# Performance work log

Hardware: AMD Instinct MI355X
Metric: run time of the kernel (lower is better)

## Reference

```python
import jax, jax.numpy as jnp
import numpy as np

LOG2 = float(np.log(2.0))
E, G, F, C = 500000, 64, 128, 4

def shifted_softplus(x):
    return jax.nn.softplus(x) - LOG2

def setup_inputs() -> dict:
    key = jax.random.key(0)
    ks = jax.random.split(key, 6)
    return {
        "edge_attr": jax.random.normal(ks[0], (E, G), dtype=jnp.float32),
        "colors": jax.random.randint(ks[1], (E,), 0, C),
        "W1": jax.random.normal(ks[2], (C, G, F), dtype=jnp.float32) * (1.0 / np.sqrt(G)),
        "b1": jax.random.normal(ks[3], (C, F), dtype=jnp.float32) * 0.01,
        "W2": jax.random.normal(ks[4], (C, F, F), dtype=jnp.float32) * (1.0 / np.sqrt(F)),
        "b2": jax.random.normal(ks[5], (C, F), dtype=jnp.float32) * 0.01,
    }

def reference(edge_attr, colors, W1, b1, W2, b2):
    # Apply every color-expert MLP to all edges, then select per-edge expert output.
    # Faithful to the torch loop: out[colors==i] = mlp_i(edge_attr[colors==i]).
    # h: [C, E, F]
    h = jnp.einsum('eg,cgf->cef', edge_attr, W1) + b1[:, None, :]
    h = shifted_softplus(h)
    y = jnp.einsum('cef,cfh->ceh', h, W2) + b2[:, None, :]  # [C, E, F]
    out = y[colors, jnp.arange(E)]  # [E, F] select each edge's own color expert
    return out
```

## Files before the change

kernel.cpp:

```cpp
#include <hip/hip_runtime.h>
#include <hip/hip_bf16.h>

#define G_DIM 64
#define F_DIM 128
#define C_DIM 4
#define NB    512

#define META_COUNTS 0
#define META_BASES  4
#define META_TSTART 9
#define BH_OFF      32
#define IDX_OFF     (32 + NB*C_DIM)

typedef __bf16 bf16x8 __attribute__((ext_vector_type(8)));
typedef float  f32x4  __attribute__((ext_vector_type(4)));

__device__ inline unsigned short f2bf(float f) {
    union { float f; unsigned u; } v; v.f = f;
    unsigned r = v.u + 0x7FFFu + ((v.u >> 16) & 1u);
    return (unsigned short)(r >> 16);
}

__device__ inline float ssp(float x) {
    float t = __expf(-fabsf(x));
    return fmaxf(x, 0.f) + __logf(1.f + t) - 0.69314718055994531f;
}

__global__ void k_prep1(const int* __restrict__ colors, int E, int CH,
                        unsigned* __restrict__ bh,
                        const float* __restrict__ W1, const float* __restrict__ W2,
                        unsigned short* __restrict__ w1t, unsigned short* __restrict__ w2t) {
    int tid = threadIdx.x;
    if (blockIdx.x < NB) {
        __shared__ unsigned h[C_DIM];
        if (tid < C_DIM) h[tid] = 0;
        __syncthreads();
        int lo = blockIdx.x * CH, hi = lo + CH; if (hi > E) hi = E;
        int lane = tid & 63;
        for (int i0 = lo; i0 < hi; i0 += 256) {
            int i = i0 + tid;
            int c = (i < hi) ? colors[i] : -1;
#pragma unroll
            for (int cc = 0; cc < C_DIM; ++cc) {
                unsigned long long m = __ballot(c == cc);
                if (lane == 0 && m) atomicAdd(&h[cc], (unsigned)__popcll(m));
            }
        }
        __syncthreads();
        if (tid < C_DIM) bh[blockIdx.x * C_DIM + tid] = h[tid];
    } else {
        int i = (blockIdx.x - NB) * 256 + tid;
        if (i < C_DIM * F_DIM * G_DIM) {
            int k = i % G_DIM, n = (i / G_DIM) % F_DIM, c = i / (G_DIM * F_DIM);
            w1t[i] = f2bf(W1[(c * G_DIM + k) * F_DIM + n]);
        }
        if (i < C_DIM * F_DIM * F_DIM) {
            int k = i % F_DIM, n = (i / F_DIM) % F_DIM, c = i / (F_DIM * F_DIM);
            w2t[i] = f2bf(W2[(c * F_DIM + k) * F_DIM + n]);
        }
    }
}

__global__ void k_prep2(const int* __restrict__ colors, int E, int CH,
                        const unsigned* __restrict__ bh, unsigned* __restrict__ meta,
                        int* __restrict__ idx) {
    __shared__ unsigned cur[C_DIM], tmpb[C_DIM], tot[C_DIM];
    int tid = threadIdx.x, w = tid >> 6, lane = tid & 63;

    unsigned run = 0;
    for (int b0 = 0; b0 < NB; b0 += 64) {
        int b = b0 + lane;
        unsigned v = bh[b * C_DIM + w];
        unsigned s = v;
#pragma unroll
        for (int d = 1; d < 64; d <<= 1) {
            unsigned t = __shfl_up(s, d, 64);
            if (lane >= d) s += t;
        }
        if (b == (int)blockIdx.x) tmpb[w] = run + s - v;
        run += __shfl(s, 63, 64);
    }
    if (lane == 0) tot[w] = run;
    __syncthreads();
    if (blockIdx.x == 0 && tid == 0) {
        unsigned bsum = 0, tsum = 0;
#pragma unroll
        for (int c = 0; c < C_DIM; ++c) {
            meta[META_BASES + c] = bsum;
            meta[META_COUNTS + c] = tot[c];
            meta[META_TSTART + c] = tsum;
            bsum += tot[c];
            tsum += (tot[c] + 63) >> 6;
        }
        meta[META_BASES + C_DIM] = bsum;
        meta[META_TSTART + C_DIM] = tsum;
    }
    if (lane == 0) {
        unsigned cb = 0;
        for (int c = 0; c < w; ++c) cb += tot[c];
        cur[w] = tmpb[w] + cb;
    }
    __syncthreads();

    int lo = blockIdx.x * CH, hi = lo + CH; if (hi > E) hi = E;
    for (int i0 = lo; i0 < hi; i0 += 256) {
        int i = i0 + tid;
        int c = (i < hi) ? colors[i] : -1;
#pragma unroll
        for (int cc = 0; cc < C_DIM; ++cc) {
            unsigned long long m = __ballot(c == cc);
            if (!m) continue;
            int leader = __ffsll(m) - 1;
            unsigned base = 0;
            if (lane == leader) base = atomicAdd(&cur[cc], (unsigned)__popcll(m));
            base = __shfl(base, leader, 64);
            if (c == cc) {
                unsigned off = __popcll(m & ((1ull << lane) - 1ull));
                idx[base + off] = i;
            }
        }
    }
}

__global__ __launch_bounds__(256, 6) void mlp_main(
    const float* __restrict__ ea, const float* __restrict__ b1,
    const float* __restrict__ b2, const unsigned short* __restrict__ w1t,
    const unsigned short* __restrict__ w2t, const unsigned* __restrict__ meta,
    const int* __restrict__ idx, float* __restrict__ out) {
    __shared__ __align__(16) unsigned short A[64][72];
    __shared__ __align__(16) unsigned short H[64][136];
    __shared__ int rowmap[64];

    unsigned b = blockIdx.x;
    if (b >= meta[META_TSTART + C_DIM]) return;
    int c = 0;
    if (b >= meta[META_TSTART + 1]) c = 1;
    if (b >= meta[META_TSTART + 2]) c = 2;
    if (b >= meta[META_TSTART + 3]) c = 3;
    int t = (int)(b - meta[META_TSTART + c]);
    int segBase = (int)meta[META_BASES + c];
    int segCnt  = (int)meta[META_COUNTS + c];
    int row0 = t * 64;
    int nrows = segCnt - row0; if (nrows > 64) nrows = 64;

    int tid = threadIdx.x;
    if (tid < 64) rowmap[tid] = (tid < nrows) ? idx[segBase + row0 + tid] : -1;
    __syncthreads();

    {
        int r = tid >> 2, q = tid & 3;
        int e = rowmap[r];
        unsigned short tmp[16];
        if (e >= 0) {
            const float4* src = (const float4*)(ea + (size_t)e * G_DIM + q * 16);
#pragma unroll
            for (int i = 0; i < 4; ++i) {
                float4 v = src[i];
                tmp[i * 4 + 0] = f2bf(v.x); tmp[i * 4 + 1] = f2bf(v.y);
                tmp[i * 4 + 2] = f2bf(v.z); tmp[i * 4 + 3] = f2bf(v.w);
            }
        } else {
#pragma unroll
            for (int i = 0; i < 16; ++i) tmp[i] = 0;
        }
        *(uint4*)&A[r][q * 16]     = *(uint4*)&tmp[0];
        *(uint4*)&A[r][q * 16 + 8] = *(uint4*)&tmp[8];
    }

    int w = tid >> 6, lane = tid & 63;
    int l15 = lane & 15, l4 = lane >> 4;

    bf16x8 fB1[2][2]; float bias1[2];
#pragma unroll
    for (int nt = 0; nt < 2; ++nt) {
        int n = w * 32 + nt * 16 + l15;
        bias1[nt] = b1[c * F_DIM + n];
#pragma unroll
        for (int ks = 0; ks < 2; ++ks)
            fB1[nt][ks] = *(const bf16x8*)(w1t + ((size_t)(c * F_DIM + n) * G_DIM + ks * 32 + l4 * 8));
    }
    __syncthreads();

    f32x4 acc[4][2];
#pragma unroll
    for (int mt = 0; mt < 4; ++mt)
#pragma unroll
        for (int nt = 0; nt < 2; ++nt) acc[mt][nt] = (f32x4){0.f, 0.f, 0.f, 0.f};
#pragma unroll
    for (int ks = 0; ks < 2; ++ks) {
#pragma unroll
        for (int mt = 0; mt < 4; ++mt) {
            bf16x8 a = *(const bf16x8*)&A[mt * 16 + l15][ks * 32 + l4 * 8];
            acc[mt][0] = __builtin_amdgcn_mfma_f32_16x16x32_bf16(a, fB1[0][ks], acc[mt][0], 0, 0, 0);
            acc[mt][1] = __builtin_amdgcn_mfma_f32_16x16x32_bf16(a, fB1[1][ks], acc[mt][1], 0, 0, 0);
        }
    }

#pragma unroll
    for (int mt = 0; mt < 4; ++mt)
#pragma unroll
        for (int nt = 0; nt < 2; ++nt)
#pragma unroll
            for (int r = 0; r < 4; ++r) {
                float v = acc[mt][nt][r] + bias1[nt];
                H[mt * 16 + l4 * 4 + r][w * 32 + nt * 16 + l15] = f2bf(ssp(v));
            }

    bf16x8 fB2[2][4]; float bias2[2];
#pragma unroll
    for (int nt = 0; nt < 2; ++nt) {
        int n = w * 32 + nt * 16 + l15;
        bias2[nt] = b2[c * F_DIM + n];
#pragma unroll
        for (int ks = 0; ks < 4; ++ks)
            fB2[nt][ks] = *(const bf16x8*)(w2t + ((size_t)(c * F_DIM + n) * F_DIM + ks * 32 + l4 * 8));
    }
    __syncthreads();

#pragma unroll
    for (int mt = 0; mt < 4; ++mt)
#pragma unroll
        for (int nt = 0; nt < 2; ++nt) acc[mt][nt] = (f32x4){0.f, 0.f, 0.f, 0.f};
#pragma unroll
    for (int ks = 0; ks < 4; ++ks) {
#pragma unroll
        for (int mt = 0; mt < 4; ++mt) {
            bf16x8 a = *(const bf16x8*)&H[mt * 16 + l15][ks * 32 + l4 * 8];
            acc[mt][0] = __builtin_amdgcn_mfma_f32_16x16x32_bf16(a, fB2[0][ks], acc[mt][0], 0, 0, 0);
            acc[mt][1] = __builtin_amdgcn_mfma_f32_16x16x32_bf16(a, fB2[1][ks], acc[mt][1], 0, 0, 0);
        }
    }

#pragma unroll
    for (int mt = 0; mt < 4; ++mt) {
#pragma unroll
        for (int r = 0; r < 4; ++r) {
            int e = rowmap[mt * 16 + l4 * 4 + r];
            if (e >= 0) {
                float* p = out + (size_t)e * F_DIM + w * 32 + l15;
                __builtin_nontemporal_store(acc[mt][0][r] + bias2[0], p);
                __builtin_nontemporal_store(acc[mt][1][r] + bias2[1], p + 16);
            }
        }
    }
}

__global__ void fallback(const float* __restrict__ ea, const int* __restrict__ colors,
                         const float* __restrict__ W1, const float* __restrict__ b1,
                         const float* __restrict__ W2, const float* __restrict__ b2,
                         float* __restrict__ out, int E) {
    __shared__ float sh[4][F_DIM + G_DIM];
    int w = threadIdx.x >> 6, lane = threadIdx.x & 63;
    int e = blockIdx.x * 4 + w;
    bool valid = (e < E);
    int ec = valid ? e : 0;
    int c = colors[ec];
    float* hv = sh[w];
    float* av = sh[w] + F_DIM;
    av[lane] = ea[(size_t)ec * G_DIM + lane];
    __syncthreads();
    for (int f = lane; f < F_DIM; f += 64) {
        float s = b1[c * F_DIM + f];
        for (int g = 0; g < G_DIM; ++g) s += av[g] * W1[(c * G_DIM + g) * F_DIM + f];
        hv[f] = ssp(s);
    }
    __syncthreads();
    for (int f = lane; f < F_DIM; f += 64) {
        float s = b2[c * F_DIM + f];
        for (int k = 0; k < F_DIM; ++k) s += hv[k] * W2[(c * F_DIM + k) * F_DIM + f];
        if (valid) out[(size_t)e * F_DIM + f] = s;
    }
}

extern "C" void kernel_launch(void* const* d_in, const int* in_sizes, int n_in,
                              void* d_out, int out_size, void* d_ws, size_t ws_size,
                              hipStream_t stream) {
    const float* ea     = (const float*)d_in[0];
    const int*   colors = (const int*)d_in[1];
    const float* W1     = (const float*)d_in[2];
    const float* b1     = (const float*)d_in[3];
    const float* W2     = (const float*)d_in[4];
    const float* b2     = (const float*)d_in[5];
    float* out = (float*)d_out;
    int E = in_sizes[1];

    size_t need = (size_t)(IDX_OFF + E) * 4 +
                  (size_t)(C_DIM * F_DIM * G_DIM + C_DIM * F_DIM * F_DIM) * 2;
    if (ws_size < need) {
        int blocks = (E + 3) / 4;
        fallback<<<blocks, 256, 0, stream>>>(ea, colors, W1, b1, W2, b2, out, E);
        return;
    }

    unsigned* meta = (unsigned*)d_ws;
    unsigned* bh   = (unsigned*)d_ws + BH_OFF;
    int* idx = (int*)d_ws + IDX_OFF;
    unsigned short* w1t = (unsigned short*)((char*)d_ws + (size_t)(IDX_OFF + E) * 4);
    unsigned short* w2t = w1t + C_DIM * F_DIM * G_DIM;

    int CH = (E + NB - 1) / NB;
    k_prep1<<<NB + 256, 256, 0, stream>>>(colors, E, CH, bh, W1, W2, w1t, w2t);
    k_prep2<<<NB, 256, 0, stream>>>(colors, E, CH, bh, meta, idx);
    int g = (E + 63) / 64 + C_DIM;
    mlp_main<<<g, 256, 0, stream>>>(ea, b1, b2, w1t, w2t, meta, idx, out);
}
```

Before: 92.24 us.

## Give each wave its own 16-row tile and drop block barriers and shared A staging

Changes the work split so each wave owns 16 rows across all 128 output features instead of 32 columns across all 64 rows. The A fragment is loaded from global straight into registers, and each wave keeps a private H slice, so the rowmap and A shared tiles and all __syncthreads go away. The cost is that every wave now loads the full W1 and W2 slices per tile (four times the weight traffic per block, mostly cache hits), and launch bounds drop from 6 to 4 blocks to leave more registers.

After: 212.4 us. 130% more time.

```diff
diff --git a/kernel.cpp b/kernel.cpp
--- a/kernel.cpp
+++ b/kernel.cpp
@@ -122,14 +122,12 @@
     }
 }
 
-__global__ __launch_bounds__(256, 6) void mlp_main(
+__global__ __launch_bounds__(256, 4) void mlp_main(
     const float* __restrict__ ea, const float* __restrict__ b1,
     const float* __restrict__ b2, const unsigned short* __restrict__ w1t,
     const unsigned short* __restrict__ w2t, const unsigned* __restrict__ meta,
     const int* __restrict__ idx, float* __restrict__ out) {
-    __shared__ __align__(16) unsigned short A[64][72];
-    __shared__ __align__(16) unsigned short H[64][136];
-    __shared__ int rowmap[64];
+    __shared__ __align__(16) unsigned short H[4][16][136];
 
     unsigned b = blockIdx.x;
     if (b >= meta[META_TSTART + C_DIM]) return;
@@ -141,105 +139,90 @@
     int segBase = (int)meta[META_BASES + c];
     int segCnt  = (int)meta[META_COUNTS + c];
     int row0 = t * 64;
-    int nrows = segCnt - row0; if (nrows > 64) nrows = 64;
-
-    int tid = threadIdx.x;
-    if (tid < 64) rowmap[tid] = (tid < nrows) ? idx[segBase + row0 + tid] : -1;
-    __syncthreads();
-
+
+    int tid = threadIdx.x, w = tid >> 6, lane = tid & 63;
+    int l15 = lane & 15, l4 = lane >> 4;
+
+    int rloc = w * 16 + l15;
+    bool av = rloc < (segCnt - row0);
+    int e_a = av ? idx[segBase + row0 + rloc] : -1;
+    int e_safe = av ? e_a : 0;
+
+    int es[4];
+#pragma unroll
+    for (int r = 0; r < 4; ++r) es[r] = __shfl(e_a, l4 * 4 + r, 64);
+
+    bf16x8 aF[2];
     {
-        int r = tid >> 2, q = tid & 3;
-        int e = rowmap[r];
-        unsigned short tmp[16];
-        if (e >= 0) {
-            const float4* src = (const float4*)(ea + (size_t)e * G_DIM + q * 16);
-#pragma unroll
-            for (int i = 0; i < 4; ++i) {
-                float4 v = src[i];
-                tmp[i * 4 + 0] = f2bf(v.x); tmp[i * 4 + 1] = f2bf(v.y);
-                tmp[i * 4 + 2] = f2bf(v.z); tmp[i * 4 + 3] = f2bf(v.w);
-            }
-        } else {
-#pragma unroll
-            for (int i = 0; i < 16; ++i) tmp[i] = 0;
-        }
-        *(uint4*)&A[r][q * 16]     = *(uint4*)&tmp[0];
-        *(uint4*)&A[r][q * 16 + 8] = *(uint4*)&tmp[8];
-    }
-
-    int w = tid >> 6, lane = tid & 63;
-    int l15 = lane & 15, l4 = lane >> 4;
-
-    bf16x8 fB1[2][2]; float bias1[2];
-#pragma unroll
-    for (int nt = 0; nt < 2; ++nt) {
-        int n = w * 32 + nt * 16 + l15;
-        bias1[nt] = b1[c * F_DIM + n];
-#pragma unroll
-        for (int ks = 0; ks < 2; ++ks)
-            fB1[nt][ks] = *(const bf16x8*)(w1t + ((size_t)(c * F_DIM + n) * G_DIM + ks * 32 + l4 * 8));
-    }
-    __syncthreads();
-
-    f32x4 acc[4][2];
-#pragma unroll
-    for (int mt = 0; mt < 4; ++mt)
-#pragma unroll
-        for (int nt = 0; nt < 2; ++nt) acc[mt][nt] = (f32x4){0.f, 0.f, 0.f, 0.f};
-#pragma unroll
-    for (int ks = 0; ks < 2; ++ks) {
-#pragma unroll
-        for (int mt = 0; mt < 4; ++mt) {
-            bf16x8 a = *(const bf16x8*)&A[mt * 16 + l15][ks * 32 + l4 * 8];
-            acc[mt][0] = __builtin_amdgcn_mfma_f32_16x16x32_bf16(a, fB1[0][ks], acc[mt][0], 0, 0, 0);
-            acc[mt][1] = __builtin_amdgcn_mfma_f32_16x16x32_bf16(a, fB1[1][ks], acc[mt][1], 0, 0, 0);
-        }
-    }
-
-#pragma unroll
-    for (int mt = 0; mt < 4; ++mt)
-#pragma unroll
-        for (int nt = 0; nt < 2; ++nt)
+        const float* src = ea + (size_t)e_safe * G_DIM + l4 * 8;
+#pragma unroll
+        for (int ks = 0; ks < 2; ++ks) {
+            float4 v0 = *(const float4*)(src + ks * 32);
+            float4 v1 = *(const float4*)(src + ks * 32 + 4);
+            union { bf16x8 b; unsigned short u[8]; } tv;
+            tv.u[0] = f2bf(v0.x); tv.u[1] = f2bf(v0.y);
+            tv.u[2] = f2bf(v0.z); tv.u[3] = f2bf(v0.w);
+            tv.u[4] = f2bf(v1.x); tv.u[5] = f2bf(v1.y);
+            tv.u[6] = f2bf(v1.z); tv.u[7] = f2bf(v1.w);
+            aF[ks] = tv.b;
+        }
+    }
+
+#pragma unroll
+    for (int nh = 0; nh < 2; ++nh) {
+        f32x4 acc[4];
+#pragma unroll
+        for (int nt = 0; nt < 4; ++nt) acc[nt] = (f32x4){0.f, 0.f, 0.f, 0.f};
+#pragma unroll
+        for (int nt = 0; nt < 4; ++nt) {
+            int n = nh * 64 + nt * 16 + l15;
+            const unsigned short* wp = w1t + (size_t)(c * F_DIM + n) * G_DIM + l4 * 8;
+            bf16x8 fb0 = *(const bf16x8*)(wp);
+            bf16x8 fb1 = *(const bf16x8*)(wp + 32);
+            acc[nt] = __builtin_amdgcn_mfma_f32_16x16x32_bf16(aF[0], fb0, acc[nt], 0, 0, 0);
+            acc[nt] = __builtin_amdgcn_mfma_f32_16x16x32_bf16(aF[1], fb1, acc[nt], 0, 0, 0);
+        }
+#pragma unroll
+        for (int nt = 0; nt < 4; ++nt) {
+            int n = nh * 64 + nt * 16 + l15;
+            float bias = b1[c * F_DIM + n];
+#pragma unroll
+            for (int r = 0; r < 4; ++r)
+                H[w][l4 * 4 + r][n] = f2bf(ssp(acc[nt][r] + bias));
+        }
+    }
+
+    asm volatile("s_waitcnt lgkmcnt(0)" ::: "memory");
+
+    bf16x8 ha[4];
+#pragma unroll
+    for (int ks = 0; ks < 4; ++ks)
+        ha[ks] = *(const bf16x8*)&H[w][l15][ks * 32 + l4 * 8];
+
+#pragma unroll
+    for (int nh = 0; nh < 2; ++nh) {
+        f32x4 acc[4];
+#pragma unroll
+        for (int nt = 0; nt < 4; ++nt) acc[nt] = (f32x4){0.f, 0.f, 0.f, 0.f};
+#pragma unroll
+        for (int nt = 0; nt < 4; ++nt) {
+            int n = nh * 64 + nt * 16 + l15;
+            const unsigned short* wp = w2t + (size_t)(c * F_DIM + n) * F_DIM + l4 * 8;
+#pragma unroll
+            for (int ks = 0; ks < 4; ++ks) {
+                bf16x8 fb = *(const bf16x8*)(wp + ks * 32);
+                acc[nt] = __builtin_amdgcn_mfma_f32_16x16x32_bf16(ha[ks], fb, acc[nt], 0, 0, 0);
+            }
+        }
+#pragma unroll
+        for (int nt = 0; nt < 4; ++nt) {
+            int n = nh * 64 + nt * 16 + l15;
+            float bias = b2[c * F_DIM + n];
 #pragma unroll
             for (int r = 0; r < 4; ++r) {
-                float v = acc[mt][nt][r] + bias1[nt];
-                H[mt * 16 + l4 * 4 + r][w * 32 + nt * 16 + l15] = f2bf(ssp(v));
-            }
-
-    bf16x8 fB2[2][4]; float bias2[2];
-#pragma unroll
-    for (int nt = 0; nt < 2; ++nt) {
-        int n = w * 32 + nt * 16 + l15;
-        bias2[nt] = b2[c * F_DIM + n];
-#pragma unroll
-        for (int ks = 0; ks < 4; ++ks)
-            fB2[nt][ks] = *(const bf16x8*)(w2t + ((size_t)(c * F_DIM + n) * F_DIM + ks * 32 + l4 * 8));
-    }
-    __syncthreads();
-
-#pragma unroll
-    for (int mt = 0; mt < 4; ++mt)
-#pragma unroll
-        for (int nt = 0; nt < 2; ++nt) acc[mt][nt] = (f32x4){0.f, 0.f, 0.f, 0.f};
-#pragma unroll
-    for (int ks = 0; ks < 4; ++ks) {
-#pragma unroll
-        for (int mt = 0; mt < 4; ++mt) {
-            bf16x8 a = *(const bf16x8*)&H[mt * 16 + l15][ks * 32 + l4 * 8];
-            acc[mt][0] = __builtin_amdgcn_mfma_f32_16x16x32_bf16(a, fB2[0][ks], acc[mt][0], 0, 0, 0);
-            acc[mt][1] = __builtin_amdgcn_mfma_f32_16x16x32_bf16(a, fB2[1][ks], acc[mt][1], 0, 0, 0);
-        }
-    }
-
-#pragma unroll
-    for (int mt = 0; mt < 4; ++mt) {
-#pragma unroll
-        for (int r = 0; r < 4; ++r) {
-            int e = rowmap[mt * 16 + l4 * 4 + r];
-            if (e >= 0) {
-                float* p = out + (size_t)e * F_DIM + w * 32 + l15;
-                __builtin_nontemporal_store(acc[mt][0][r] + bias2[0], p);
-                __builtin_nontemporal_store(acc[mt][1][r] + bias2[1], p + 16);
+                if (es[r] >= 0)
+                    __builtin_nontemporal_store(acc[nt][r] + bias,
+                                                out + (size_t)es[r] * F_DIM + n);
             }
         }
     }
```
